# Performance work log

Measured on AMD Instinct MI355X. Metric: run time of the kernel, lower is better.

## Reference

```python
import jax, jax.numpy as jnp
import numpy as np

INHIBITION_INCREASE = 5.0
DECAY_RATE = 100.0
DECAY_SIGMA = 5.0
DT = 0.001
DT_SQRT = float(np.sqrt(DT))


def setup_inputs() -> dict:
    key = jax.random.key(0)
    k1, k2 = jax.random.split(key)
    inputs = jax.random.normal(k1, (8192, 2048), dtype=jnp.float32)
    inhibition = jax.random.normal(k2, (8192, 1), dtype=jnp.float32)
    return {"inputs": inputs, "inhibition": inhibition}


def reference(inputs, inhibition):
    key = jax.random.key(42)
    kn, ku, kc = jax.random.split(key, 3)
    # inhibition decay + diffusion noise (Euler-Maruyama step)
    inhib = (1.0 - DECAY_RATE * DT) * inhibition + DECAY_SIGMA * DT_SQRT * jax.random.normal(kn, inhibition.shape, dtype=inhibition.dtype)
    # instantaneous firing rates, clipped for numerical safety
    rates = jnp.clip(jnp.exp(inputs - inhib), 1e-20, 1e20)  # [B, N]
    total_rate = jnp.sum(rates, axis=-1, keepdims=True)      # [B, 1]
    rand_val = jax.random.uniform(ku, total_rate.shape, dtype=total_rate.dtype)
    spike_occurred = rand_val < DT * total_rate               # [B, 1] bool
    # categorical over rates == categorical with logits log(rates)
    spike_location = jax.random.categorical(kc, jnp.log(rates), axis=-1)  # [B]
    out_spike_locations = jax.nn.one_hot(spike_location, rates.shape[-1], dtype=inputs.dtype)  # [B, N]
    out_spikes = out_spike_locations * spike_occurred.astype(inputs.dtype)  # [B, N]
    inhib = inhib + jnp.max(out_spikes, axis=-1, keepdims=True) * INHIBITION_INCREASE
    return out_spikes, inhib
```

## Files before the change

### kernel.cpp

```cpp
#include <hip/hip_runtime.h>
#include <cstdint>
#include <cmath>

#define N_ROWS 8192
#define N_COLS 2048
#define OUT_SPIKES_ELEMS (N_ROWS * N_COLS)

__host__ __device__ inline uint32_t rotl32(uint32_t x, int d) {
#if defined(__HIP_DEVICE_COMPILE__)
  return __builtin_amdgcn_alignbit(x, x, 32u - (uint32_t)d);
#else
  return (x << d) | (x >> (32 - d));
#endif
}

__host__ __device__ inline void threefry2x32(uint32_t k0, uint32_t k1,
                                             uint32_t x0, uint32_t x1,
                                             uint32_t& o0, uint32_t& o1) {
  const uint32_t ks2 = k0 ^ k1 ^ 0x1BD11BDAu;
  x0 += k0; x1 += k1;
#define TFR(r) { x0 += x1; x1 = rotl32(x1, (r)); x1 ^= x0; }
  TFR(13) TFR(15) TFR(26) TFR(6)
  x0 += k1; x1 += ks2 + 1u;
  TFR(17) TFR(29) TFR(16) TFR(24)
  x0 += ks2; x1 += k0 + 2u;
  TFR(13) TFR(15) TFR(26) TFR(6)
  x0 += k0; x1 += k1 + 3u;
  TFR(17) TFR(29) TFR(16) TFR(24)
  x0 += k1; x1 += ks2 + 4u;
  TFR(13) TFR(15) TFR(26) TFR(6)
  x0 += ks2; x1 += k0 + 5u;
#undef TFR
  o0 = x0; o1 = x1;
}

__device__ inline uint32_t random_bits32(uint32_t k0, uint32_t k1, uint32_t j) {
  uint32_t o0, o1;
  threefry2x32(k0, k1, 0u, j, o0, o1);
  return o0 ^ o1;
}

__device__ inline float unit_from_bits(uint32_t bits) {
  return __uint_as_float((bits >> 9) | 0x3f800000u) - 1.0f;
}

__device__ inline float xla_erfinv(float x) {
  float w = -log1pf(__fmul_rn(-x, x));
  float p;
  if (w < 5.0f) {
    w = __fadd_rn(w, -2.5f);
    p = 2.81022636e-08f;
    p = __fadd_rn(3.43273939e-07f,  __fmul_rn(p, w));
    p = __fadd_rn(-3.5233877e-06f,  __fmul_rn(p, w));
    p = __fadd_rn(-4.39150654e-06f, __fmul_rn(p, w));
    p = __fadd_rn(0.00021858087f,   __fmul_rn(p, w));
    p = __fadd_rn(-0.00125372503f,  __fmul_rn(p, w));
    p = __fadd_rn(-0.00417768164f,  __fmul_rn(p, w));
    p = __fadd_rn(0.246640727f,     __fmul_rn(p, w));
    p = __fadd_rn(1.50140941f,      __fmul_rn(p, w));
  } else {
    w = __fadd_rn(sqrtf(w), -3.0f);
    p = -0.000200214257f;
    p = __fadd_rn(0.000100950558f,  __fmul_rn(p, w));
    p = __fadd_rn(0.00134934322f,   __fmul_rn(p, w));
    p = __fadd_rn(-0.00367342844f,  __fmul_rn(p, w));
    p = __fadd_rn(0.00573950773f,   __fmul_rn(p, w));
    p = __fadd_rn(-0.0076224613f,   __fmul_rn(p, w));
    p = __fadd_rn(0.00943887047f,   __fmul_rn(p, w));
    p = __fadd_rn(1.00167406f,      __fmul_rn(p, w));
    p = __fadd_rn(2.83297682f,      __fmul_rn(p, w));
  }
  return __fmul_rn(p, x);
}

__device__ inline float normal_from_bits(uint32_t bits) {
  const float lo = -0.99999994f;
  float unit = unit_from_bits(bits);
  float t = __fadd_rn(__fmul_rn(unit, 2.0f), lo);
  t = fmaxf(lo, t);
  return __fmul_rn(1.4142135623730951f, xla_erfinv(t));
}

__device__ inline float compute_ih(const float* __restrict__ inhibition,
                                   int row, float csig,
                                   uint32_t kn0, uint32_t kn1) {
  float nrm = normal_from_bits(random_bits32(kn0, kn1, (uint32_t)row));
  return __fadd_rn(__fmul_rn(0.9f, inhibition[row]), __fmul_rn(csig, nrm));
}

__global__ __launch_bounds__(256, 6) void spike_kernel(
    const float* __restrict__ inputs, const float* __restrict__ inhibition,
    float* __restrict__ out, float csig,
    uint32_t kn0, uint32_t kn1, uint32_t ku0, uint32_t ku1,
    uint32_t kc0, uint32_t kc1) {
  const int row = blockIdx.x;
  const int tid = threadIdx.x;
  const int wid = tid >> 6;
  const float tiny = 1.17549435e-38f;
  const float ln2 = 0.69314718055994531f;
  const float log2e = 1.4426950408889634f;

  __shared__ uint32_t lbits[8 * 256];
  __shared__ float    lvhat[8 * 256];
  __shared__ double s_sum[4];
  __shared__ float  s_cv[4];
  __shared__ int    s_ci[4];
  __shared__ int    s_final[2];

  const float* rowp = inputs + (size_t)row * N_COLS;
  const float4* rowp4 = reinterpret_cast<const float4*>(rowp);
  float4 a0 = rowp4[tid];
  float4 a1 = rowp4[tid + 256];
  float xv[8] = {a0.x, a0.y, a0.z, a0.w, a1.x, a1.y, a1.z, a1.w};

  float vmaxA = -INFINITY, vmaxB = -INFINITY;
  double tsA = 0.0, tsB = 0.0;
  const uint32_t jbase = (uint32_t)(row * N_COLS + 4 * tid);

#pragma unroll
  for (int i8 = 0; i8 < 8; ++i8) {
    const uint32_t j = jbase + (uint32_t)((i8 & 3) + 1024 * (i8 >> 2));
    uint32_t bits = random_bits32(kc0, kc1, j);
    float u = unit_from_bits(bits);
    float t = __fadd_rn(u, tiny);
    float w = __fmul_rn(-ln2, __log2f(t));
    float g = __fmul_rn(-ln2, __log2f(w));
    float v = __fadd_rn(g, xv[i8]);
    lbits[i8 * 256 + tid] = bits;
    lvhat[i8 * 256 + tid] = v;
    double e = (double)__builtin_amdgcn_exp2f(__fmul_rn(xv[i8], log2e));
    if (i8 & 1) { vmaxB = fmaxf(vmaxB, v); tsB += e; }
    else        { vmaxA = fmaxf(vmaxA, v); tsA += e; }
  }
  const float tmax = fmaxf(vmaxA, vmaxB);
  float vmax = tmax;
  double tsum = tsA + tsB;

#pragma unroll
  for (int off = 32; off > 0; off >>= 1) {
    tsum += __shfl_xor(tsum, off);
    vmax = fmaxf(vmax, __shfl_xor(vmax, off));
  }
  const float thrM = __fsub_rn(vmax, 1e-3f);

  float cval = -INFINITY;
  int   cidx = 0x7fffffff;
  if (tmax >= thrM) {
    float ih = compute_ih(inhibition, row, csig, kn0, kn1);
#pragma unroll
    for (int i8 = 0; i8 < 8; ++i8) {
      float vh = lvhat[i8 * 256 + tid];
      if (vh >= thrM) {
        int col = 4 * tid + 1024 * (i8 >> 2) + (i8 & 3);
        uint32_t bits = lbits[i8 * 256 + tid];
        float t = __fadd_rn(unit_from_bits(bits), tiny);
        float g = -logf(-logf(t));
        float x = __fsub_rn(rowp[col], ih);
        float v = __fadd_rn(g, x);
        if (v > cval || (v == cval && col < cidx)) { cval = v; cidx = col; }
      }
    }
  }

#pragma unroll
  for (int off = 32; off > 0; off >>= 1) {
    float ov = __shfl_xor(cval, off);
    int   oi = __shfl_xor(cidx, off);
    if (ov > cval || (ov == cval && oi < cidx)) { cval = ov; cidx = oi; }
  }

  if ((tid & 63) == 0) { s_sum[wid] = tsum; s_cv[wid] = cval; s_ci[wid] = cidx; }
  __syncthreads();

  if (tid == 0) {
    double T = s_sum[0] + s_sum[1] + s_sum[2] + s_sum[3];
    float bv = s_cv[0];
    int   bi = s_ci[0];
    for (int w = 1; w < 4; ++w) {
      if (s_cv[w] > bv || (s_cv[w] == bv && s_ci[w] < bi)) { bv = s_cv[w]; bi = s_ci[w]; }
    }
    float ih = compute_ih(inhibition, row, csig, kn0, kn1);
    double total = T * (double)expf(-ih);
    float urand = unit_from_bits(random_bits32(ku0, ku1, (uint32_t)row));
    float thr = __fmul_rn(0.001f, (float)total);
    int spike = (urand < thr) ? 1 : 0;
    s_final[0] = bi;
    s_final[1] = spike;
    out[OUT_SPIKES_ELEMS + row] = spike ? __fadd_rn(ih, 5.0f) : ih;
  }
  __syncthreads();

  const int bi = s_final[0];
  const int spike = s_final[1];
  float* orow = out + (size_t)row * N_COLS;
#pragma unroll
  for (int ch = 0; ch < 2; ++ch) {
    const int col = 4 * tid + 1024 * ch;
    float4 z = make_float4(0.f, 0.f, 0.f, 0.f);
    if (spike && bi >= col && bi < col + 4) {
      (&z.x)[bi - col] = 1.0f;
    }
    *reinterpret_cast<float4*>(orow + col) = z;
  }
}

extern "C" void kernel_launch(void* const* d_in, const int* in_sizes, int n_in,
                              void* d_out, int out_size, void* d_ws, size_t ws_size,
                              hipStream_t stream) {
  const float* inputs     = (const float*)d_in[0];
  const float* inhibition = (const float*)d_in[1];
  float* out = (float*)d_out;

  uint32_t kn0, kn1, ku0, ku1, kc0, kc1;
  threefry2x32(0u, 42u, 0u, 0u, kn0, kn1);
  threefry2x32(0u, 42u, 0u, 1u, ku0, ku1);
  threefry2x32(0u, 42u, 0u, 2u, kc0, kc1);

  const float csig = (float)(5.0 * sqrt(0.001));

  dim3 grid(N_ROWS), block(256);
  hipLaunchKernelGGL(spike_kernel, grid, block, 0, stream,
                     inputs, inhibition, out, csig,
                     kn0, kn1, ku0, ku1, kc0, kc1);
}
```

Measured before the change: 58.09 us.

## Use 512-thread blocks with 4 elements per thread, register-held candidates, float sums

The row is split across 512 threads, each handling one float4 instead of two. Per-element random bits and perturbed logits now stay in registers, so the LDS staging arrays go away. The row sum of exponentials is accumulated in float rather than double. Together these aim to raise parallelism and cut LDS traffic and FP64 work, at the risk of slightly different rounding in the spike-threshold sum and a larger cross-wave reduction.

```diff
diff --git a/kernel.cpp b/kernel.cpp
--- a/kernel.cpp
+++ b/kernel.cpp
@@ -88,7 +88,7 @@
   return __fadd_rn(__fmul_rn(0.9f, inhibition[row]), __fmul_rn(csig, nrm));
 }
 
-__global__ __launch_bounds__(256, 6) void spike_kernel(
+__global__ __launch_bounds__(512, 8) void spike_kernel(
     const float* __restrict__ inputs, const float* __restrict__ inhibition,
     float* __restrict__ out, float csig,
     uint32_t kn0, uint32_t kn1, uint32_t ku0, uint32_t ku1,
@@ -100,41 +100,37 @@
   const float ln2 = 0.69314718055994531f;
   const float log2e = 1.4426950408889634f;
 
-  __shared__ uint32_t lbits[8 * 256];
-  __shared__ float    lvhat[8 * 256];
-  __shared__ double s_sum[4];
-  __shared__ float  s_cv[4];
-  __shared__ int    s_ci[4];
-  __shared__ int    s_final[2];
+  __shared__ float s_sum[8];
+  __shared__ float s_cv[8];
+  __shared__ int   s_ci[8];
+  __shared__ int   s_final[2];
 
   const float* rowp = inputs + (size_t)row * N_COLS;
-  const float4* rowp4 = reinterpret_cast<const float4*>(rowp);
-  float4 a0 = rowp4[tid];
-  float4 a1 = rowp4[tid + 256];
-  float xv[8] = {a0.x, a0.y, a0.z, a0.w, a1.x, a1.y, a1.z, a1.w};
-
+  float4 a = reinterpret_cast<const float4*>(rowp)[tid];
+  float xv[4] = {a.x, a.y, a.z, a.w};
+
+  uint32_t bits4[4];
+  float vhat4[4];
   float vmaxA = -INFINITY, vmaxB = -INFINITY;
-  double tsA = 0.0, tsB = 0.0;
+  float tsA = 0.0f, tsB = 0.0f;
   const uint32_t jbase = (uint32_t)(row * N_COLS + 4 * tid);
 
 #pragma unroll
-  for (int i8 = 0; i8 < 8; ++i8) {
-    const uint32_t j = jbase + (uint32_t)((i8 & 3) + 1024 * (i8 >> 2));
-    uint32_t bits = random_bits32(kc0, kc1, j);
+  for (int k = 0; k < 4; ++k) {
+    uint32_t bits = random_bits32(kc0, kc1, jbase + (uint32_t)k);
     float u = unit_from_bits(bits);
     float t = __fadd_rn(u, tiny);
     float w = __fmul_rn(-ln2, __log2f(t));
     float g = __fmul_rn(-ln2, __log2f(w));
-    float v = __fadd_rn(g, xv[i8]);
-    lbits[i8 * 256 + tid] = bits;
-    lvhat[i8 * 256 + tid] = v;
-    double e = (double)__builtin_amdgcn_exp2f(__fmul_rn(xv[i8], log2e));
-    if (i8 & 1) { vmaxB = fmaxf(vmaxB, v); tsB += e; }
-    else        { vmaxA = fmaxf(vmaxA, v); tsA += e; }
+    float v = __fadd_rn(g, xv[k]);
+    bits4[k] = bits; vhat4[k] = v;
+    float e = __builtin_amdgcn_exp2f(__fmul_rn(xv[k], log2e));
+    if (k & 1) { vmaxB = fmaxf(vmaxB, v); tsB += e; }
+    else       { vmaxA = fmaxf(vmaxA, v); tsA += e; }
   }
   const float tmax = fmaxf(vmaxA, vmaxB);
   float vmax = tmax;
-  double tsum = tsA + tsB;
+  float tsum = tsA + tsB;
 
 #pragma unroll
   for (int off = 32; off > 0; off >>= 1) {
@@ -148,12 +144,10 @@
   if (tmax >= thrM) {
     float ih = compute_ih(inhibition, row, csig, kn0, kn1);
 #pragma unroll
-    for (int i8 = 0; i8 < 8; ++i8) {
-      float vh = lvhat[i8 * 256 + tid];
-      if (vh >= thrM) {
-        int col = 4 * tid + 1024 * (i8 >> 2) + (i8 & 3);
-        uint32_t bits = lbits[i8 * 256 + tid];
-        float t = __fadd_rn(unit_from_bits(bits), tiny);
+    for (int k = 0; k < 4; ++k) {
+      if (vhat4[k] >= thrM) {
+        int col = 4 * tid + k;
+        float t = __fadd_rn(unit_from_bits(bits4[k]), tiny);
         float g = -logf(-logf(t));
         float x = __fsub_rn(rowp[col], ih);
         float v = __fadd_rn(g, x);
@@ -173,14 +167,17 @@
   __syncthreads();
 
   if (tid == 0) {
-    double T = s_sum[0] + s_sum[1] + s_sum[2] + s_sum[3];
+    float T = 0.0f;
+#pragma unroll
+    for (int w = 0; w < 8; ++w) T += s_sum[w];
     float bv = s_cv[0];
     int   bi = s_ci[0];
-    for (int w = 1; w < 4; ++w) {
+#pragma unroll
+    for (int w = 1; w < 8; ++w) {
       if (s_cv[w] > bv || (s_cv[w] == bv && s_ci[w] < bi)) { bv = s_cv[w]; bi = s_ci[w]; }
     }
     float ih = compute_ih(inhibition, row, csig, kn0, kn1);
-    double total = T * (double)expf(-ih);
+    double total = (double)T * (double)expf(-ih);
     float urand = unit_from_bits(random_bits32(ku0, ku1, (uint32_t)row));
     float thr = __fmul_rn(0.001f, (float)total);
     int spike = (urand < thr) ? 1 : 0;
@@ -192,16 +189,12 @@
 
   const int bi = s_final[0];
   const int spike = s_final[1];
-  float* orow = out + (size_t)row * N_COLS;
-#pragma unroll
-  for (int ch = 0; ch < 2; ++ch) {
-    const int col = 4 * tid + 1024 * ch;
-    float4 z = make_float4(0.f, 0.f, 0.f, 0.f);
-    if (spike && bi >= col && bi < col + 4) {
-      (&z.x)[bi - col] = 1.0f;
-    }
-    *reinterpret_cast<float4*>(orow + col) = z;
-  }
+  const int col = 4 * tid;
+  float4 z = make_float4(0.f, 0.f, 0.f, 0.f);
+  if (spike && bi >= col && bi < col + 4) {
+    (&z.x)[bi - col] = 1.0f;
+  }
+  *reinterpret_cast<float4*>(out + (size_t)row * N_COLS + col) = z;
 }
 
 extern "C" void kernel_launch(void* const* d_in, const int* in_sizes, int n_in,
@@ -218,7 +211,7 @@
 
   const float csig = (float)(5.0 * sqrt(0.001));
 
-  dim3 grid(N_ROWS), block(256);
+  dim3 grid(N_ROWS), block(512);
   hipLaunchKernelGGL(spike_kernel, grid, block, 0, stream,
                      inputs, inhibition, out, csig,
                      kn0, kn1, ku0, ku1, kc0, kc1);
```

New measurement: 76.66 us. +32.0%, slower.

## Precompute per-row inhibition and uniforms in a setup kernel; use float sums

Applied to the files above, without the earlier changes.

Adds a small pre-kernel that computes each row's noisy inhibition, exp(-ih) and the spike uniform into workspace, so the main kernel no longer runs the erfinv and extra threefry work serially on thread 0. It also switches the rate sum from double to float accumulation, packs bits and the Gumbel value into one uint2 shared stash, and folds the Gumbel negation into an fma. The costs are an extra kernel launch and the loss of double-precision accumulation in the total-rate sum, which could change spike decisions right at the threshold.

```diff
diff --git a/kernel.cpp b/kernel.cpp
--- a/kernel.cpp
+++ b/kernel.cpp
@@ -81,31 +81,33 @@
   return __fmul_rn(1.4142135623730951f, xla_erfinv(t));
 }
 
-__device__ inline float compute_ih(const float* __restrict__ inhibition,
-                                   int row, float csig,
-                                   uint32_t kn0, uint32_t kn1) {
-  float nrm = normal_from_bits(random_bits32(kn0, kn1, (uint32_t)row));
-  return __fadd_rn(__fmul_rn(0.9f, inhibition[row]), __fmul_rn(csig, nrm));
+__global__ __launch_bounds__(256) void row_setup_kernel(
+    const float* __restrict__ inhibition, float* __restrict__ ws, float csig,
+    uint32_t kn0, uint32_t kn1, uint32_t ku0, uint32_t ku1) {
+  int r = blockIdx.x * 256 + threadIdx.x;
+  if (r >= N_ROWS) return;
+  float nrm = normal_from_bits(random_bits32(kn0, kn1, (uint32_t)r));
+  float ih = __fadd_rn(__fmul_rn(0.9f, inhibition[r]), __fmul_rn(csig, nrm));
+  float pre = expf(-ih);
+  float ur  = unit_from_bits(random_bits32(ku0, ku1, (uint32_t)r));
+  reinterpret_cast<float4*>(ws)[r] = make_float4(ih, pre, ur, 0.0f);
 }
 
 __global__ __launch_bounds__(256, 6) void spike_kernel(
-    const float* __restrict__ inputs, const float* __restrict__ inhibition,
-    float* __restrict__ out, float csig,
-    uint32_t kn0, uint32_t kn1, uint32_t ku0, uint32_t ku1,
-    uint32_t kc0, uint32_t kc1) {
+    const float* __restrict__ inputs, const float* __restrict__ ws,
+    float* __restrict__ out, uint32_t kc0, uint32_t kc1) {
   const int row = blockIdx.x;
   const int tid = threadIdx.x;
   const int wid = tid >> 6;
   const float tiny = 1.17549435e-38f;
-  const float ln2 = 0.69314718055994531f;
+  const float nln2 = -0.69314718055994531f;
   const float log2e = 1.4426950408889634f;
 
-  __shared__ uint32_t lbits[8 * 256];
-  __shared__ float    lvhat[8 * 256];
-  __shared__ double s_sum[4];
-  __shared__ float  s_cv[4];
-  __shared__ int    s_ci[4];
-  __shared__ int    s_final[2];
+  __shared__ uint2 stash[8 * 256];
+  __shared__ float s_sum[4];
+  __shared__ float s_cv[4];
+  __shared__ int   s_ci[4];
+  __shared__ int   s_final[2];
 
   const float* rowp = inputs + (size_t)row * N_COLS;
   const float4* rowp4 = reinterpret_cast<const float4*>(rowp);
@@ -114,7 +116,7 @@
   float xv[8] = {a0.x, a0.y, a0.z, a0.w, a1.x, a1.y, a1.z, a1.w};
 
   float vmaxA = -INFINITY, vmaxB = -INFINITY;
-  double tsA = 0.0, tsB = 0.0;
+  float tsA = 0.0f, tsB = 0.0f;
   const uint32_t jbase = (uint32_t)(row * N_COLS + 4 * tid);
 
 #pragma unroll
@@ -123,18 +125,16 @@
     uint32_t bits = random_bits32(kc0, kc1, j);
     float u = unit_from_bits(bits);
     float t = __fadd_rn(u, tiny);
-    float w = __fmul_rn(-ln2, __log2f(t));
-    float g = __fmul_rn(-ln2, __log2f(w));
-    float v = __fadd_rn(g, xv[i8]);
-    lbits[i8 * 256 + tid] = bits;
-    lvhat[i8 * 256 + tid] = v;
-    double e = (double)__builtin_amdgcn_exp2f(__fmul_rn(xv[i8], log2e));
+    float m = __log2f(t);
+    float v = fmaf(nln2, __log2f(-m), xv[i8]);
+    stash[i8 * 256 + tid] = make_uint2(bits, __float_as_uint(v));
+    float e = __builtin_amdgcn_exp2f(__fmul_rn(xv[i8], log2e));
     if (i8 & 1) { vmaxB = fmaxf(vmaxB, v); tsB += e; }
     else        { vmaxA = fmaxf(vmaxA, v); tsA += e; }
   }
   const float tmax = fmaxf(vmaxA, vmaxB);
   float vmax = tmax;
-  double tsum = tsA + tsB;
+  float tsum = tsA + tsB;
 
 #pragma unroll
   for (int off = 32; off > 0; off >>= 1) {
@@ -146,14 +146,13 @@
   float cval = -INFINITY;
   int   cidx = 0x7fffffff;
   if (tmax >= thrM) {
-    float ih = compute_ih(inhibition, row, csig, kn0, kn1);
+    float ih = ws[4 * row];
 #pragma unroll
     for (int i8 = 0; i8 < 8; ++i8) {
-      float vh = lvhat[i8 * 256 + tid];
-      if (vh >= thrM) {
+      uint2 s = stash[i8 * 256 + tid];
+      if (__uint_as_float(s.y) >= thrM) {
         int col = 4 * tid + 1024 * (i8 >> 2) + (i8 & 3);
-        uint32_t bits = lbits[i8 * 256 + tid];
-        float t = __fadd_rn(unit_from_bits(bits), tiny);
+        float t = __fadd_rn(unit_from_bits(s.x), tiny);
         float g = -logf(-logf(t));
         float x = __fsub_rn(rowp[col], ih);
         float v = __fadd_rn(g, x);
@@ -173,20 +172,19 @@
   __syncthreads();
 
   if (tid == 0) {
-    double T = s_sum[0] + s_sum[1] + s_sum[2] + s_sum[3];
+    float T = s_sum[0] + s_sum[1] + s_sum[2] + s_sum[3];
     float bv = s_cv[0];
     int   bi = s_ci[0];
     for (int w = 1; w < 4; ++w) {
       if (s_cv[w] > bv || (s_cv[w] == bv && s_ci[w] < bi)) { bv = s_cv[w]; bi = s_ci[w]; }
     }
-    float ih = compute_ih(inhibition, row, csig, kn0, kn1);
-    double total = T * (double)expf(-ih);
-    float urand = unit_from_bits(random_bits32(ku0, ku1, (uint32_t)row));
+    float4 wsd = reinterpret_cast<const float4*>(ws)[row];
+    double total = (double)T * (double)wsd.y;
     float thr = __fmul_rn(0.001f, (float)total);
-    int spike = (urand < thr) ? 1 : 0;
+    int spike = (wsd.z < thr) ? 1 : 0;
     s_final[0] = bi;
     s_final[1] = spike;
-    out[OUT_SPIKES_ELEMS + row] = spike ? __fadd_rn(ih, 5.0f) : ih;
+    out[OUT_SPIKES_ELEMS + row] = spike ? __fadd_rn(wsd.x, 5.0f) : wsd.x;
   }
   __syncthreads();
 
@@ -210,6 +208,7 @@
   const float* inputs     = (const float*)d_in[0];
   const float* inhibition = (const float*)d_in[1];
   float* out = (float*)d_out;
+  float* ws  = (float*)d_ws;
 
   uint32_t kn0, kn1, ku0, ku1, kc0, kc1;
   threefry2x32(0u, 42u, 0u, 0u, kn0, kn1);
@@ -218,8 +217,8 @@
 
   const float csig = (float)(5.0 * sqrt(0.001));
 
-  dim3 grid(N_ROWS), block(256);
-  hipLaunchKernelGGL(spike_kernel, grid, block, 0, stream,
-                     inputs, inhibition, out, csig,
-                     kn0, kn1, ku0, ku1, kc0, kc1);
-}
+  hipLaunchKernelGGL(row_setup_kernel, dim3(N_ROWS / 256), dim3(256), 0, stream,
+                     inhibition, ws, csig, kn0, kn1, ku0, ku1);
+  hipLaunchKernelGGL(spike_kernel, dim3(N_ROWS), dim3(256), 0, stream,
+                     inputs, ws, out, kc0, kc1);
+}
```

New measurement: 57.25 us. About the same (-1.4%).
